# Kernel optimization log

Measured on AMD Instinct MI355X. Metric: run time of the kernel, lower is better.

The kernel has to match this reference:

```python
import jax, jax.numpy as jnp
import numpy as np

B, H, W, C = 16, 64, 64, 192
NH, WS, SHIFT = 6, 8, 4          # heads, window size, shift (window//2)
DEPTH, MLP_R = 2, 4
N = WS * WS                      # tokens per window = 64
HD = C // NH                     # head dim = 32
SCALE = HD ** -0.5
TBL = (2 * WS - 1) ** 2          # relative-bias table size = 225
NW = (H // WS) * (W // WS)       # windows per image = 64


def _rel_pos_index():
    coords = np.stack(np.meshgrid(np.arange(WS), np.arange(WS), indexing='ij')).reshape(2, -1)
    rel = (coords[:, :, None] - coords[:, None, :]).transpose(1, 2, 0)
    rel[..., 0] += WS - 1
    rel[..., 1] += WS - 1
    rel[..., 0] *= 2 * WS - 1
    return jnp.asarray(rel.sum(-1))  # [N, N] int


def _attn_mask():
    # Swin shifted-window mask: region ids then pairwise -100 where ids differ.
    img = np.zeros((H, W))
    sl = (slice(0, -WS), slice(-WS, -SHIFT), slice(-SHIFT, None))
    cnt = 0
    for hs in sl:
        for ws in sl:
            img[hs, ws] = cnt
            cnt += 1
    mw = img.reshape(H // WS, WS, W // WS, WS).transpose(0, 2, 1, 3).reshape(-1, N)
    diff = mw[:, None, :] - mw[:, :, None]
    return jnp.asarray(np.where(diff != 0, -100.0, 0.0).astype(np.float32))  # [NW, N, N]


REL_IDX = _rel_pos_index()
ATTN_MASK = _attn_mask()


def _ln(x, g, b, eps=1e-5):
    mu = x.mean(-1, keepdims=True)
    var = ((x - mu) ** 2).mean(-1, keepdims=True)
    return (x - mu) * jax.lax.rsqrt(var + eps) * g + b


def setup_inputs() -> dict:
    key = jax.random.key(0)
    ks = jax.random.split(key, 8)
    s = 0.02
    return {
        'x': jax.random.normal(ks[0], (B, H * W, C), jnp.float32),
        'norm1_g': jnp.ones((DEPTH, C)), 'norm1_b': jnp.zeros((DEPTH, C)),
        'qkv_w': jax.random.normal(ks[1], (DEPTH, 3 * C, C)) * s,
        'qkv_b': jnp.zeros((DEPTH, 3 * C)),
        'bias_table': jax.random.normal(ks[2], (DEPTH, TBL, NH)) * s,
        'proj_w': jax.random.normal(ks[3], (DEPTH, C, C)) * s,
        'proj_b': jnp.zeros((DEPTH, C)),
        'norm2_g': jnp.ones((DEPTH, C)), 'norm2_b': jnp.zeros((DEPTH, C)),
        'fc1_w': jax.random.normal(ks[4], (DEPTH, MLP_R * C, C)) * s,
        'fc1_b': jnp.zeros((DEPTH, MLP_R * C)),
        'fc2_w': jax.random.normal(ks[5], (DEPTH, C, MLP_R * C)) * s,
        'fc2_b': jnp.zeros((DEPTH, C)),
    }


def _block(x, shift, n1g, n1b, qw, qb, tbl, pw, pb, n2g, n2b, f1w, f1b, f2w, f2b):
    shortcut = x
    y = _ln(x, n1g, n1b).reshape(B, H, W, C)
    if shift > 0:
        y = jnp.roll(y, (-shift, -shift), axis=(1, 2))
    # window partition -> [B*NW, N, C]
    win = y.reshape(B, H // WS, WS, W // WS, WS, C).transpose(0, 1, 3, 2, 4, 5).reshape(-1, N, C)
    qkv = (win @ qw.T + qb).reshape(-1, N, 3, NH, HD).transpose(2, 0, 3, 1, 4)
    q, k, v = qkv[0] * SCALE, qkv[1], qkv[2]          # each [B*NW, NH, N, HD]
    attn = jnp.einsum('bhnd,bhmd->bhnm', q, k)
    attn = attn + tbl[REL_IDX].transpose(2, 0, 1)[None]  # relative position bias
    if shift > 0:
        attn = (attn.reshape(B, NW, NH, N, N) + ATTN_MASK[None, :, None]).reshape(-1, NH, N, N)
    attn = jax.nn.softmax(attn, axis=-1)
    o = jnp.einsum('bhnm,bhmd->bhnd', attn, v).transpose(0, 2, 1, 3).reshape(-1, N, C)
    o = o @ pw.T + pb
    # window reverse
    y = o.reshape(B, H // WS, W // WS, WS, WS, C).transpose(0, 1, 3, 2, 4, 5).reshape(B, H, W, C)
    if shift > 0:
        y = jnp.roll(y, (shift, shift), axis=(1, 2))
    x = shortcut + y.reshape(B, H * W, C)
    h = _ln(x, n2g, n2b)
    h = jax.nn.gelu(h @ f1w.T + f1b, approximate=False)  # torch nn.GELU = exact erf
    return x + (h @ f2w.T + f2b)


def reference(x, norm1_g, norm1_b, qkv_w, qkv_b, bias_table, proj_w, proj_b,
              norm2_g, norm2_b, fc1_w, fc1_b, fc2_w, fc2_b):
    for i in range(DEPTH):
        shift = 0 if i % 2 == 0 else SHIFT
        x = _block(x, shift, norm1_g[i], norm1_b[i], qkv_w[i], qkv_b[i], bias_table[i],
                   proj_w[i], proj_b[i], norm2_g[i], norm2_b[i],
                   fc1_w[i], fc1_b[i], fc2_w[i], fc2_b[i])
    return x
```

## Files before the change

### kernel.cpp

```cpp
#include <hip/hip_runtime.h>
#include <hip/hip_bf16.h>
#include <math.h>

typedef __hip_bfloat16 bf16;
typedef short bf16x8 __attribute__((ext_vector_type(8)));
typedef short s16x4 __attribute__((ext_vector_type(4)));
typedef float f32x4 __attribute__((ext_vector_type(4)));

#define TOKENS 65536
#define C_ 192

__device__ __forceinline__ float b2f(bf16 v){ return __bfloat162float(v); }
__device__ __forceinline__ bf16 f2b(float v){ return __float2bfloat16(v); }
__device__ __forceinline__ short f2s(float v){
  bf16 b = __float2bfloat16(v);
  union { bf16 b; short s; } u; u.b = b; return u.s;
}
__device__ __forceinline__ float s2f(short s){
  union { unsigned u; float f; } c; c.u = ((unsigned)(unsigned short)s) << 16; return c.f;
}

__global__ void detect_k(const unsigned* __restrict__ g, int* __restrict__ flag){
  *flag = (g[0] == 0x3F800000u) ? 1 : 0;
}
__global__ void xconv_k(const void* __restrict__ x, float* __restrict__ y, int n,
                        const int* __restrict__ flag){
  int i = blockIdx.x*blockDim.x + threadIdx.x;
  if (i >= n) return;
  if (*flag) y[i] = ((const float*)x)[i];
  else       y[i] = b2f(((const bf16*)x)[i]);
}
struct WPtrs { const void* p[13]; };
__global__ void wconv_all_k(WPtrs wp, const int* __restrict__ offs, const int* __restrict__ lens,
                            bf16* __restrict__ dst, int total, const int* __restrict__ flag){
  int i = blockIdx.x*blockDim.x + threadIdx.x;
  if (i >= total) return;
  int t = 0;
  while (t < 12 && i >= offs[t+1]) t++;
  int j = i - offs[t];
  if (j >= lens[t]) return;
  if (*flag) dst[i] = f2b(((const float*)wp.p[t])[j]);
  else       dst[i] = ((const bf16*)wp.p[t])[j];
}
__global__ void outconv_k(const float* __restrict__ x, void* __restrict__ y, int n,
                          const int* __restrict__ flag){
  int i = blockIdx.x*blockDim.x + threadIdx.x;
  if (i >= n) return;
  if (*flag) ((float*)y)[i] = x[i];
  else       ((bf16*)y)[i]  = f2b(x[i]);
}

__global__ void bias_setup_k(const bf16* __restrict__ bt, float* __restrict__ biasF){
  int idx = blockIdx.x*blockDim.x + threadIdx.x;
  if (idx >= 2*6*64*64) return;
  int v = idx & 63;
  int lane = (idx >> 6) & 63;
  int rest = idx >> 12;
  int head = rest % 6, dd = rest / 6;
  int jt = v >> 4, it = (v >> 2) & 3, r = v & 3;
  int quad = lane >> 4, lr = lane & 15;
  int j = jt*16 + quad*4 + r;
  int i = it*16 + lr;
  int rel = ((i>>3) - (j>>3) + 7)*15 + ((i&7) - (j&7) + 7);
  biasF[idx] = b2f(bt[(dd*225 + rel)*6 + head]);
}

__global__ void mlp_repack_k(const bf16* __restrict__ f1w, const bf16* __restrict__ f2w,
                             bf16* __restrict__ w1p, bf16* __restrict__ w2p){
  int id = blockIdx.x*blockDim.x + threadIdx.x;
  if (id >= 589824) return;
  int arr = id / 294912;
  int r = id % 294912;
  int d = r / 147456;
  int e = r % 147456;
  int j = e & 7, lane = (e >> 3) & 63, frag = e >> 9;
  int lr = lane & 15, quad = lane >> 4;
  if (arr == 0){
    int ks = frag % 6, t = frag / 6;
    int mh = t & 1, cc = t >> 1;
    w1p[(size_t)d*147456 + e] =
        f1w[(size_t)d*147456 + (size_t)(cc*32 + mh*16 + lr)*192 + ks*32 + quad*8 + j];
  } else {
    int ct = frag % 12, cc = frag / 12;
    w2p[(size_t)d*147456 + e] =
        f2w[(size_t)d*147456 + (size_t)(ct*16 + lr)*768 + cc*32 + quad*8 + j];
  }
}

__global__ __launch_bounds__(768, 1) void attn_fused_k(float* __restrict__ xres,
    const bf16* __restrict__ n1g, const bf16* __restrict__ n1b,
    const bf16* __restrict__ qw, const bf16* __restrict__ qb,
    const bf16* __restrict__ pw, const bf16* __restrict__ pb,
    const float* __restrict__ biasF, int shift)
{
  extern __shared__ char smem[];
  short* xo = (short*)smem;
  int win = blockIdx.x;
  int tid = threadIdx.x;
  int wave = tid >> 6, lane = tid & 63;
  int quad = lane >> 4, lr = lane & 15;
  int head = wave >> 1, half = wave & 1;
  int b_ = win >> 6, wl = win & 63, wh = wl >> 3, wwi = wl & 7;
  short* kh  = (short*)(smem + 25600 + head*17408);
  short* vth = kh + 2048;
  short* qP  = vth + 2304;

  int c0 = lane*3;
  float g0 = b2f(n1g[c0]), g1 = b2f(n1g[c0+1]), g2 = b2f(n1g[c0+2]);
  float e0 = b2f(n1b[c0]), e1 = b2f(n1b[c0+1]), e2 = b2f(n1b[c0+2]);
  #pragma unroll
  for (int p = 0; p < 6; p++){
    int tok = p*12 + wave;
    if (tok < 64){
      int hh = (wh*8 + (tok>>3) + shift) & 63, ww = (wwi*8 + (tok&7) + shift) & 63;
      const float* rowp = xres + ((size_t)(b_<<12) + (hh<<6) + ww)*C_;
      float v0 = rowp[c0], v1 = rowp[c0+1], v2 = rowp[c0+2];
      float s = v0+v1+v2;
      #pragma unroll
      for (int off=32; off; off>>=1) s += __shfl_xor(s, off);
      float mu = s * (1.0f/192.0f);
      float d0=v0-mu, d1=v1-mu, d2=v2-mu;
      float q = d0*d0+d1*d1+d2*d2;
      #pragma unroll
      for (int off=32; off; off>>=1) q += __shfl_xor(q, off);
      float rstd = rsqrtf(q*(1.0f/192.0f) + 1e-5f);
      xo[tok*200 + c0]   = f2s(d0*rstd*g0 + e0);
      xo[tok*200 + c0+1] = f2s(d1*rstd*g1 + e1);
      xo[tok*200 + c0+2] = f2s(d2*rstd*g2 + e2);
    }
  }
  __syncthreads();

  const short* qwd = (const short*)qw;
  #pragma unroll
  for (int cc = 0; cc < 3; cc++){
    int nbase = cc*192 + head*32;
    f32x4 acc[2][2];
    #pragma unroll
    for (int mt = 0; mt < 2; mt++)
      #pragma unroll
      for (int nt = 0; nt < 2; nt++) acc[mt][nt] = (f32x4){0.f,0.f,0.f,0.f};
    #pragma unroll
    for (int ks = 0; ks < 6; ks++){
      bf16x8 af[2], bx[2];
      #pragma unroll
      for (int mt = 0; mt < 2; mt++)
        af[mt] = *(const bf16x8*)(qwd + (size_t)(nbase + mt*16 + lr)*192 + ks*32 + quad*8);
      #pragma unroll
      for (int nt = 0; nt < 2; nt++)
        bx[nt] = *(const bf16x8*)&xo[((2*half + nt)*16 + lr)*200 + ks*32 + quad*8];
      #pragma unroll
      for (int mt = 0; mt < 2; mt++)
        #pragma unroll
        for (int nt = 0; nt < 2; nt++)
          acc[mt][nt] = __builtin_amdgcn_mfma_f32_16x16x32_bf16(af[mt], bx[nt], acc[mt][nt], 0, 0, 0);
    }
    #pragma unroll
    for (int mt = 0; mt < 2; mt++){
      float bv[4];
      #pragma unroll
      for (int r = 0; r < 4; r++) bv[r] = b2f(qb[nbase + mt*16 + quad*4 + r]);
      #pragma unroll
      for (int nt = 0; nt < 2; nt++){
        int tok = (2*half + nt)*16 + lr;
        if (cc == 0){
          s16x4 pk;
          #pragma unroll
          for (int r = 0; r < 4; r++) pk[r] = f2s((acc[mt][nt][r] + bv[r]) * 0.17677669529663689f);
          *(s16x4*)&qP[tok*32 + mt*16 + quad*4] = pk;
        } else if (cc == 1){
          s16x4 pk;
          #pragma unroll
          for (int r = 0; r < 4; r++) pk[r] = f2s(acc[mt][nt][r] + bv[r]);
          *(s16x4*)&kh[tok*32 + mt*16 + quad*4] = pk;
        } else {
          #pragma unroll
          for (int r = 0; r < 4; r++)
            vth[(mt*16 + quad*4 + r)*72 + tok] = f2s(acc[mt][nt][r] + bv[r]);
        }
      }
    }
  }
  __syncthreads();

  bf16x8 ak[4], bq[2];
  #pragma unroll
  for (int jt = 0; jt < 4; jt++) ak[jt] = *(const bf16x8*)&kh[(jt*16 + lr)*32 + quad*8];
  #pragma unroll
  for (int it = 0; it < 2; it++)
    bq[it] = *(const bf16x8*)&qP[((2*half + it)*16 + lr)*32 + quad*8];
  __syncthreads();

  f32x4 S[4][2];
  #pragma unroll
  for (int jt = 0; jt < 4; jt++)
    #pragma unroll
    for (int it = 0; it < 2; it++) S[jt][it] = (f32x4){0.f,0.f,0.f,0.f};
  #pragma unroll
  for (int jt = 0; jt < 4; jt++)
    #pragma unroll
    for (int it = 0; it < 2; it++)
      S[jt][it] = __builtin_amdgcn_mfma_f32_16x16x32_bf16(ak[jt], bq[it], S[jt][it], 0, 0, 0);

  const f32x4* bm = (const f32x4*)(biasF + ((size_t)head*64 + lane)*64);
  #pragma unroll
  for (int jt = 0; jt < 4; jt++)
    #pragma unroll
    for (int it = 0; it < 2; it++) S[jt][it] += bm[jt*4 + 2*half + it];

  if (shift){
    int idi[2];
    #pragma unroll
    for (int it = 0; it < 2; it++){
      int itg = 2*half + it;
      int hh = wh*8 + itg*2 + (lr >> 3);
      int wwc = wwi*8 + (lr & 7);
      idi[it] = (hh < 56 ? 0 : (hh < 60 ? 1 : 2))*3 + (wwc < 56 ? 0 : (wwc < 60 ? 1 : 2));
    }
    #pragma unroll
    for (int jt = 0; jt < 4; jt++)
      #pragma unroll
      for (int r = 0; r < 4; r++){
        int j = jt*16 + quad*4 + r;
        int hh = wh*8 + (j >> 3), wwc = wwi*8 + (j & 7);
        int idj = (hh < 56 ? 0 : (hh < 60 ? 1 : 2))*3 + (wwc < 56 ? 0 : (wwc < 60 ? 1 : 2));
        #pragma unroll
        for (int it = 0; it < 2; it++)
          if (idj != idi[it]) S[jt][it][r] -= 100.f;
      }
  }
  #pragma unroll
  for (int it = 0; it < 2; it++){
    float m = -1e30f;
    #pragma unroll
    for (int jt = 0; jt < 4; jt++)
      #pragma unroll
      for (int r = 0; r < 4; r++) m = fmaxf(m, S[jt][it][r]);
    m = fmaxf(m, __shfl_xor(m, 16));
    m = fmaxf(m, __shfl_xor(m, 32));
    float s = 0.f;
    #pragma unroll
    for (int jt = 0; jt < 4; jt++)
      #pragma unroll
      for (int r = 0; r < 4; r++){
        float e = __expf(S[jt][it][r] - m);
        S[jt][it][r] = e; s += e;
      }
    s += __shfl_xor(s, 16);
    s += __shfl_xor(s, 32);
    float inv = 1.0f / s;
    #pragma unroll
    for (int jt = 0; jt < 4; jt++){
      s16x4 pk;
      #pragma unroll
      for (int r = 0; r < 4; r++) pk[r] = f2s(S[jt][it][r] * inv);
      *(s16x4*)&qP[((2*half + it)*16 + lr)*68 + jt*16 + quad*4] = pk;
    }
  }
  __syncthreads();

  bf16x8 va[2][2], pv[2][2];
  #pragma unroll
  for (int mt = 0; mt < 2; mt++)
    #pragma unroll
    for (int ks = 0; ks < 2; ks++)
      va[mt][ks] = *(const bf16x8*)&vth[(mt*16 + lr)*72 + ks*32 + quad*8];
  #pragma unroll
  for (int nt = 0; nt < 2; nt++)
    #pragma unroll
    for (int ks = 0; ks < 2; ks++)
      pv[nt][ks] = *(const bf16x8*)&qP[((2*half + nt)*16 + lr)*68 + ks*32 + quad*8];

  f32x4 O[2][2];
  #pragma unroll
  for (int mt = 0; mt < 2; mt++)
    #pragma unroll
    for (int nt = 0; nt < 2; nt++) O[mt][nt] = (f32x4){0.f,0.f,0.f,0.f};
  #pragma unroll
  for (int mt = 0; mt < 2; mt++)
    #pragma unroll
    for (int nt = 0; nt < 2; nt++)
      #pragma unroll
      for (int ks = 0; ks < 2; ks++)
        O[mt][nt] = __builtin_amdgcn_mfma_f32_16x16x32_bf16(va[mt][ks], pv[nt][ks], O[mt][nt], 0, 0, 0);

  #pragma unroll
  for (int mt = 0; mt < 2; mt++)
    #pragma unroll
    for (int nt = 0; nt < 2; nt++){
      s16x4 pk;
      #pragma unroll
      for (int r = 0; r < 4; r++) pk[r] = f2s(O[mt][nt][r]);
      *(s16x4*)&xo[((2*half + nt)*16 + lr)*200 + head*32 + mt*16 + quad*4] = pk;
    }
  __syncthreads();

  int wm = wave / 6, wn = wave % 6;
  f32x4 po[2][2];
  #pragma unroll
  for (int mt = 0; mt < 2; mt++)
    #pragma unroll
    for (int nt = 0; nt < 2; nt++) po[mt][nt] = (f32x4){0.f,0.f,0.f,0.f};
  const short* pwd = (const short*)pw;
  #pragma unroll
  for (int ks = 0; ks < 6; ks++){
    bf16x8 ao[2], bw[2];
    #pragma unroll
    for (int mt = 0; mt < 2; mt++)
      ao[mt] = *(const bf16x8*)&xo[(wm*32 + mt*16 + lr)*200 + ks*32 + quad*8];
    #pragma unroll
    for (int nt = 0; nt < 2; nt++)
      bw[nt] = *(const bf16x8*)(pwd + (size_t)(wn*32 + nt*16 + lr)*192 + ks*32 + quad*8);
    #pragma unroll
    for (int mt = 0; mt < 2; mt++)
      #pragma unroll
      for (int nt = 0; nt < 2; nt++)
        po[mt][nt] = __builtin_amdgcn_mfma_f32_16x16x32_bf16(ao[mt], bw[nt], po[mt][nt], 0, 0, 0);
  }
  #pragma unroll
  for (int nt = 0; nt < 2; nt++){
    int n = wn*32 + nt*16 + lr;
    float bv = b2f(pb[n]);
    #pragma unroll
    for (int mt = 0; mt < 2; mt++){
      #pragma unroll
      for (int r = 0; r < 4; r++){
        int tok = wm*32 + mt*16 + quad*4 + r;
        int hh = (wh*8 + (tok>>3) + shift) & 63, ww = (wwi*8 + (tok&7) + shift) & 63;
        float* dst = xres + ((size_t)(b_<<12) + (hh<<6) + ww)*C_ + n;
        *dst += po[mt][nt][r] + bv;
      }
    }
  }
}

__global__ __launch_bounds__(256, 4) void mlp_tlp_k(float* __restrict__ xres,
    const bf16* __restrict__ n2g, const bf16* __restrict__ n2b,
    const bf16* __restrict__ w1p, const bf16* __restrict__ f1b,
    const bf16* __restrict__ w2p, const bf16* __restrict__ f2bv)
{
  __shared__ short HsAll[4][16*36];
  int tid = threadIdx.x;
  int wave = tid >> 6, lane = tid & 63;
  int quad = lane >> 4, lr = lane & 15;
  short* Hs = HsAll[wave];
  int t0 = blockIdx.x*64 + wave*16;

  bf16x8 xh[6];
  {
    const float* rowp = xres + (size_t)(t0 + lr)*C_;
    float v[6][8];
    float s = 0.f;
    #pragma unroll
    for (int ks = 0; ks < 6; ks++){
      int cb = ks*32 + quad*8;
      #pragma unroll
      for (int j = 0; j < 8; j++){ v[ks][j] = rowp[cb+j]; s += v[ks][j]; }
    }
    s += __shfl_xor(s, 16); s += __shfl_xor(s, 32);
    float mu = s*(1.0f/192.0f);
    float q = 0.f;
    #pragma unroll
    for (int ks = 0; ks < 6; ks++)
      #pragma unroll
      for (int j = 0; j < 8; j++){ float d = v[ks][j]-mu; q += d*d; }
    q += __shfl_xor(q, 16); q += __shfl_xor(q, 32);
    float rstd = rsqrtf(q*(1.0f/192.0f) + 1e-5f);
    #pragma unroll
    for (int ks = 0; ks < 6; ks++){
      int cb = ks*32 + quad*8;
      #pragma unroll
      for (int j = 0; j < 8; j++)
        xh[ks][j] = f2s((v[ks][j]-mu)*rstd*b2f(n2g[cb+j]) + b2f(n2b[cb+j]));
    }
  }

  f32x4 acc[12];
  #pragma unroll
  for (int ct = 0; ct < 12; ct++) acc[ct] = (f32x4){0.f,0.f,0.f,0.f};

  const short* w1 = (const short*)w1p;
  const short* w2 = (const short*)w2p;

  for (int cc = 0; cc < 24; cc++){
    f32x4 hacc[2];
    hacc[0] = (f32x4){0.f,0.f,0.f,0.f};
    hacc[1] = (f32x4){0.f,0.f,0.f,0.f};
    #pragma unroll
    for (int ks = 0; ks < 6; ks++){
      bf16x8 af0 = *(const bf16x8*)(w1 + (size_t)(cc*12 + ks)*512 + lane*8);
      bf16x8 af1 = *(const bf16x8*)(w1 + (size_t)(cc*12 + 6 + ks)*512 + lane*8);
      hacc[0] = __builtin_amdgcn_mfma_f32_16x16x32_bf16(af0, xh[ks], hacc[0], 0, 0, 0);
      hacc[1] = __builtin_amdgcn_mfma_f32_16x16x32_bf16(af1, xh[ks], hacc[1], 0, 0, 0);
    }
    #pragma unroll
    for (int mh = 0; mh < 2; mh++){
      s16x4 bb = *(const s16x4*)((const short*)f1b + cc*32 + mh*16 + quad*4);
      s16x4 pk;
      #pragma unroll
      for (int r = 0; r < 4; r++){
        float x = hacc[mh][r] + s2f(bb[r]);
        float y = x*(0.7978845608f + 0.0356774081f*x*x);
        float t = __expf(2.0f*fminf(y, 9.0f));
        pk[r] = f2s(x*t/(t + 1.0f));
      }
      *(s16x4*)&Hs[lr*36 + mh*16 + quad*4] = pk;
    }
    bf16x8 ah = *(const bf16x8*)&Hs[lr*36 + quad*8];
    #pragma unroll
    for (int ct = 0; ct < 12; ct++){
      bf16x8 bw = *(const bf16x8*)(w2 + (size_t)(cc*12 + ct)*512 + lane*8);
      acc[ct] = __builtin_amdgcn_mfma_f32_16x16x32_bf16(bw, ah, acc[ct], 0, 0, 0);
    }
  }

  {
    int m = t0 + lr;
    float* rowd = xres + (size_t)m*C_;
    #pragma unroll
    for (int ct = 0; ct < 12; ct++){
      int n0 = ct*16 + quad*4;
      s16x4 bb = *(const s16x4*)((const short*)f2bv + n0);
      f32x4* dst = (f32x4*)(rowd + n0);
      f32x4 cur = *dst;
      #pragma unroll
      for (int r = 0; r < 4; r++) cur[r] += acc[ct][r] + s2f(bb[r]);
      *dst = cur;
    }
  }
}

extern "C" void kernel_launch(void* const* d_in, const int* in_sizes, int n_in,
                              void* d_out, int out_size, void* d_ws, size_t ws_size,
                              hipStream_t stream)
{
  (void)in_sizes; (void)n_in; (void)out_size;

  if (ws_size < (size_t)52117000) return;
  char* ws = (char*)d_ws;
  float* xf   = (float*)ws;
  bf16* canon = (bf16*)(ws + 50331648);
  int*  flagp = (int*)(ws + 52116608);
  float* biasF = (float*)d_out;
  bf16* w1p = (bf16*)((char*)d_out + 196608);
  bf16* w2p = (bf16*)((char*)d_out + 786432);

  static const int W_OFF[13] = {0, 384, 768, 221952, 223104, 225856, 299584,
                                299968, 300352, 300736, 595648, 597184, 892096};
  const int W_TOTAL = 892480;

  hipFuncSetAttribute((const void*)attn_fused_k,
                      hipFuncAttributeMaxDynamicSharedMemorySize, 130048);

  detect_k<<<1, 1, 0, stream>>>((const unsigned*)d_in[1], flagp);

  WPtrs wp;
  for (int i = 0; i < 13; i++) wp.p[i] = d_in[i+1];
  {
    int* meta = (int*)(ws + 52116672);
    struct Init {
      static __global__ void run(int* meta){
        const int offs[13] = {0, 384, 768, 221952, 223104, 225856, 299584,
                              299968, 300352, 300736, 595648, 597184, 892096};
        const int lens[13] = {384, 384, 221184, 1152, 2700, 73728, 384,
                              384, 384, 294912, 1536, 294912, 384};
        int i = threadIdx.x;
        if (i < 13){ meta[i] = offs[i]; meta[13+i] = lens[i]; }
      }
    };
    hipLaunchKernelGGL(Init::run, dim3(1), dim3(16), 0, stream, meta);
    wconv_all_k<<<(W_TOTAL + 255)/256, 256, 0, stream>>>(wp, meta, meta+13, canon, W_TOTAL, flagp);
  }

  const int nelem = TOKENS*C_;
  xconv_k<<<nelem/256, 256, 0, stream>>>(d_in[0], xf, nelem, flagp);

  const bf16* n1g = canon + W_OFF[0];
  const bf16* n1b = canon + W_OFF[1];
  const bf16* qw  = canon + W_OFF[2];
  const bf16* qb  = canon + W_OFF[3];
  const bf16* bt  = canon + W_OFF[4];
  const bf16* pw  = canon + W_OFF[5];
  const bf16* pb  = canon + W_OFF[6];
  const bf16* n2g = canon + W_OFF[7];
  const bf16* n2b = canon + W_OFF[8];
  const bf16* f1w = canon + W_OFF[9];
  const bf16* f1b = canon + W_OFF[10];
  const bf16* f2w = canon + W_OFF[11];
  const bf16* f2bv= canon + W_OFF[12];

  bias_setup_k<<<(2*6*64*64)/256, 256, 0, stream>>>(bt, biasF);
  mlp_repack_k<<<(589824 + 255)/256, 256, 0, stream>>>(f1w, f2w, w1p, w2p);

  for (int d = 0; d < 2; d++){
    int shift = d ? 4 : 0;
    attn_fused_k<<<1024, 768, 130048, stream>>>(xf,
        n1g + d*192, n1b + d*192, qw + d*576*192, qb + d*576,
        pw + d*192*192, pb + d*192, biasF + d*6*64*64, shift);
    mlp_tlp_k<<<1024, 256, 0, stream>>>(xf,
        n2g + d*192, n2b + d*192, w1p + d*147456, f1b + d*768,
        w2p + d*147456, f2bv + d*192);
  }
  outconv_k<<<nelem/256, 256, 0, stream>>>(xf, d_out, nelem, flagp);
}
```

Measured before the change: 629.9 us.

## Stage MLP weights cooperatively in LDS with double-buffered prefetch

After: 581.1 us. -7.7%, faster.

```diff
diff --git a/kernel.cpp b/kernel.cpp
--- a/kernel.cpp
+++ b/kernel.cpp
@@ -334,17 +334,32 @@
   }
 }
 
-__global__ __launch_bounds__(256, 4) void mlp_tlp_k(float* __restrict__ xres,
+__global__ __launch_bounds__(512, 4) void mlp_coop_k(float* __restrict__ xres,
     const bf16* __restrict__ n2g, const bf16* __restrict__ n2b,
     const bf16* __restrict__ w1p, const bf16* __restrict__ f1b,
     const bf16* __restrict__ w2p, const bf16* __restrict__ f2bv)
 {
-  __shared__ short HsAll[4][16*36];
+  __shared__ short Wst[2][24*512];
+  __shared__ short HsAll[8][16*36];
   int tid = threadIdx.x;
   int wave = tid >> 6, lane = tid & 63;
   int quad = lane >> 4, lr = lane & 15;
   short* Hs = HsAll[wave];
-  int t0 = blockIdx.x*64 + wave*16;
+  int t0 = blockIdx.x*128 + wave*16;
+
+  const short* w1 = (const short*)w1p;
+  const short* w2 = (const short*)w2p;
+
+  int f0 = wave*3;
+
+  bf16x8 rg[3];
+  #pragma unroll
+  for (int k = 0; k < 3; k++){
+    int f = f0 + k;
+    const short* g = (f < 12) ? (w1 + (size_t)f*512 + lane*8)
+                              : (w2 + (size_t)(f - 12)*512 + lane*8);
+    rg[k] = *(const bf16x8*)g;
+  }
 
   bf16x8 xh[6];
   {
@@ -375,21 +390,37 @@
     }
   }
 
+  #pragma unroll
+  for (int k = 0; k < 3; k++)
+    *(bf16x8*)&Wst[0][(f0 + k)*512 + lane*8] = rg[k];
+
   f32x4 acc[12];
   #pragma unroll
   for (int ct = 0; ct < 12; ct++) acc[ct] = (f32x4){0.f,0.f,0.f,0.f};
 
-  const short* w1 = (const short*)w1p;
-  const short* w2 = (const short*)w2p;
-
+  int cur = 0;
   for (int cc = 0; cc < 24; cc++){
+    if (cc < 23){
+      #pragma unroll
+      for (int k = 0; k < 3; k++){
+        int f = f0 + k;
+        const short* g = (f < 12) ? (w1 + (size_t)((cc+1)*12 + f)*512 + lane*8)
+                                  : (w2 + (size_t)((cc+1)*12 + (f - 12))*512 + lane*8);
+        rg[k] = *(const bf16x8*)g;
+      }
+    }
+
+    __syncthreads();
+
+    const short* rdb = &Wst[cur][0];
+
     f32x4 hacc[2];
     hacc[0] = (f32x4){0.f,0.f,0.f,0.f};
     hacc[1] = (f32x4){0.f,0.f,0.f,0.f};
     #pragma unroll
     for (int ks = 0; ks < 6; ks++){
-      bf16x8 af0 = *(const bf16x8*)(w1 + (size_t)(cc*12 + ks)*512 + lane*8);
-      bf16x8 af1 = *(const bf16x8*)(w1 + (size_t)(cc*12 + 6 + ks)*512 + lane*8);
+      bf16x8 af0 = *(const bf16x8*)&rdb[ks*512 + lane*8];
+      bf16x8 af1 = *(const bf16x8*)&rdb[(6 + ks)*512 + lane*8];
       hacc[0] = __builtin_amdgcn_mfma_f32_16x16x32_bf16(af0, xh[ks], hacc[0], 0, 0, 0);
       hacc[1] = __builtin_amdgcn_mfma_f32_16x16x32_bf16(af1, xh[ks], hacc[1], 0, 0, 0);
     }
@@ -409,9 +440,16 @@
     bf16x8 ah = *(const bf16x8*)&Hs[lr*36 + quad*8];
     #pragma unroll
     for (int ct = 0; ct < 12; ct++){
-      bf16x8 bw = *(const bf16x8*)(w2 + (size_t)(cc*12 + ct)*512 + lane*8);
+      bf16x8 bw = *(const bf16x8*)&rdb[(12 + ct)*512 + lane*8];
       acc[ct] = __builtin_amdgcn_mfma_f32_16x16x32_bf16(bw, ah, acc[ct], 0, 0, 0);
     }
+
+    if (cc < 23){
+      #pragma unroll
+      for (int k = 0; k < 3; k++)
+        *(bf16x8*)&Wst[cur ^ 1][(f0 + k)*512 + lane*8] = rg[k];
+    }
+    cur ^= 1;
   }
 
   {
@@ -422,10 +460,10 @@
       int n0 = ct*16 + quad*4;
       s16x4 bb = *(const s16x4*)((const short*)f2bv + n0);
       f32x4* dst = (f32x4*)(rowd + n0);
-      f32x4 cur = *dst;
-      #pragma unroll
-      for (int r = 0; r < 4; r++) cur[r] += acc[ct][r] + s2f(bb[r]);
-      *dst = cur;
+      f32x4 cur4 = *dst;
+      #pragma unroll
+      for (int r = 0; r < 4; r++) cur4[r] += acc[ct][r] + s2f(bb[r]);
+      *dst = cur4;
     }
   }
 }
@@ -497,7 +535,7 @@
     attn_fused_k<<<1024, 768, 130048, stream>>>(xf,
         n1g + d*192, n1b + d*192, qw + d*576*192, qb + d*576,
         pw + d*192*192, pb + d*192, biasF + d*6*64*64, shift);
-    mlp_tlp_k<<<1024, 256, 0, stream>>>(xf,
+    mlp_coop_k<<<512, 512, 0, stream>>>(xf,
         n2g + d*192, n2b + d*192, w1p + d*147456, f1b + d*768,
         w2p + d*147456, f2bv + d*192);
   }
```
